# Kernel tuning notes

Measured on AMD Instinct MI355X. Metric: run time of the kernel, lower is better.

## Reference

```python
import jax, jax.numpy as jnp
import numpy as np

N = 50000      # nodes
E = 800000     # edges (before self-loops)
F_IN = 128
H = 4          # heads
C = 64         # per-head channels
G = 64         # graphs in batch
NEG_SLOPE = 0.2


def setup_inputs() -> dict:
    key = jax.random.key(0)
    ks = jax.random.split(key, 20)
    rn = lambda k, shape, s=0.1: (jax.random.normal(k, shape, jnp.float32) * s)
    x = jax.random.normal(ks[0], (N, F_IN), jnp.float32)
    edge_index = jax.random.randint(ks[1], (2, E), 0, N, dtype=jnp.int32)
    batch = jnp.sort(jax.random.randint(ks[2], (N,), 0, G, dtype=jnp.int32))
    return {
        "x": x, "edge_index": edge_index, "batch": batch,
        # layer 0: 128 -> (4 heads x 64), concat
        "W0": rn(ks[3], (F_IN, H * C)), "a_src0": rn(ks[4], (H, C)), "a_dst0": rn(ks[5], (H, C)), "b0": jnp.zeros((H * C,), jnp.float32),
        "W1": rn(ks[6], (H * C, H * C)), "a_src1": rn(ks[7], (H, C)), "a_dst1": rn(ks[8], (H, C)), "b1": jnp.zeros((H * C,), jnp.float32),
        "W2": rn(ks[9], (H * C, C)), "a_src2": rn(ks[10], (1, C)), "a_dst2": rn(ks[11], (1, C)), "b2": jnp.zeros((C,), jnp.float32),
        "lin_w": rn(ks[12], (C, 1)), "lin_b": jnp.zeros((1,), jnp.float32),
    }


def gat_layer(h_in, src, dst, W, a_src, a_dst, b, heads, ch, concat):
    n = h_in.shape[0]
    h = (h_in @ W).reshape(n, heads, ch)                         # [N,H,C]
    e_src = jnp.sum(h * a_src[None], axis=-1)                    # [N,H]
    e_dst = jnp.sum(h * a_dst[None], axis=-1)                    # [N,H]
    e = jax.nn.leaky_relu(e_src[src] + e_dst[dst], NEG_SLOPE)    # [E,H]
    # segment softmax over incoming edges of each destination node
    m = jax.ops.segment_max(e, dst, num_segments=n)
    m = jnp.where(jnp.isneginf(m), 0.0, m)
    ex = jnp.exp(e - m[dst])
    denom = jax.ops.segment_sum(ex, dst, num_segments=n)
    alpha = ex / (denom[dst] + 1e-16)                            # [E,H]
    out = jax.ops.segment_sum(h[src] * alpha[:, :, None], dst, num_segments=n)  # [N,H,C]
    out = out.reshape(n, heads * ch) if concat else out.mean(axis=1)
    return out + b


def reference(x, edge_index, batch, W0, a_src0, a_dst0, b0, W1, a_src1, a_dst1, b1, W2, a_src2, a_dst2, b2, lin_w, lin_b):
    n = x.shape[0]
    loops = jnp.arange(n, dtype=edge_index.dtype)
    src = jnp.concatenate([edge_index[0], loops])  # PyG add_self_loops=True
    dst = jnp.concatenate([edge_index[1], loops])
    h = jax.nn.relu(gat_layer(x, src, dst, W0, a_src0, a_dst0, b0, H, C, True))
    h = jax.nn.relu(gat_layer(h, src, dst, W1, a_src1, a_dst1, b1, H, C, True))
    h = gat_layer(h, src, dst, W2, a_src2, a_dst2, b2, 1, C, False)  # [N,64]
    # global mean pool per graph
    counts = jax.ops.segment_sum(jnp.ones((n,), h.dtype), batch, num_segments=G)
    pooled = jax.ops.segment_sum(h, batch, num_segments=G) / jnp.maximum(counts, 1.0)[:, None]
    return pooled @ lin_w + lin_b  # [G,1]
```

## Files before the change

### kernel.cpp

```cpp
#include <hip/hip_runtime.h>
#include <math.h>

typedef __bf16 bf16x8 __attribute__((ext_vector_type(8)));
typedef __bf16 bf16x4 __attribute__((ext_vector_type(4)));
typedef float f32x4 __attribute__((ext_vector_type(4)));
typedef float f32x2 __attribute__((ext_vector_type(2)));
typedef unsigned int u32x2 __attribute__((ext_vector_type(2)));
typedef unsigned int u32x4 __attribute__((ext_vector_type(4)));

#define LOG2E 1.4426950408889634f

static __device__ __forceinline__ float lrelu(float e) { return e > 0.0f ? e : 0.2f * e; }
static __device__ __forceinline__ float fexp2(float x) { return __builtin_amdgcn_exp2f(x); }

static __device__ __forceinline__ void dec16(u32x4 u, float* f) {
#pragma unroll
  for (int i = 0; i < 4; i++) {
    f32x2 a = __builtin_amdgcn_cvt_pk_f32_fp8(u[i], false);
    f32x2 b = __builtin_amdgcn_cvt_pk_f32_fp8(u[i], true);
    f[i * 4 + 0] = a.x;
    f[i * 4 + 1] = a.y;
    f[i * 4 + 2] = b.x;
    f[i * 4 + 3] = b.y;
  }
}

static __device__ __forceinline__ void dec8(unsigned int lo, unsigned int hi, float* f) {
  f32x2 a = __builtin_amdgcn_cvt_pk_f32_fp8(lo, false);
  f32x2 b = __builtin_amdgcn_cvt_pk_f32_fp8(lo, true);
  f32x2 c = __builtin_amdgcn_cvt_pk_f32_fp8(hi, false);
  f32x2 d = __builtin_amdgcn_cvt_pk_f32_fp8(hi, true);
  f[0] = a.x; f[1] = a.y; f[2] = b.x; f[3] = b.y;
  f[4] = c.x; f[5] = c.y; f[6] = d.x; f[7] = d.y;
}

static __device__ __forceinline__ int cmap(int p) {
  return (p & ~63) + (p & 3) * 16 + ((p & 63) >> 2);
}

__global__ void prep_kernel(const float* __restrict__ x, __bf16* __restrict__ xb, int n4,
                            const float* __restrict__ W0, __bf16* __restrict__ Bt0,
                            const float* __restrict__ W1, __bf16* __restrict__ Bt1,
                            const float* __restrict__ W2, __bf16* __restrict__ Bt2, int FIN,
                            int* __restrict__ cnt, int n) {
  int cb = (n4 + 255) / 256;
  int b = blockIdx.x;
  if (b < cb) {
    int i = b * 256 + threadIdx.x;
    if (i < n4) {
      f32x4 v = ((const f32x4*)x)[i];
      bf16x4 o = {(__bf16)v.x, (__bf16)v.y, (__bf16)v.z, (__bf16)v.w};
      ((bf16x4*)xb)[i] = o;
    }
    return;
  }
  b -= cb;
  if (b < 256) {
    for (int k = threadIdx.x; k < FIN; k += 256) Bt0[b * FIN + k] = (__bf16)W0[k * 256 + b];
    return;
  }
  b -= 256;
  if (b < 256) {
    int k = threadIdx.x;
    Bt1[b * 256 + k] = (__bf16)W1[cmap(k) * 256 + b];
    return;
  }
  b -= 256;
  if (b < 64) {
    int k = threadIdx.x;
    Bt2[b * 256 + k] = (__bf16)W2[cmap(k) * 64 + b];
    return;
  }
  b -= 64;
  int i = b * 256 + threadIdx.x;
  if (i < n) cnt[i] = 0;
}

template <int K, int NT>
__global__ __launch_bounds__(256) void count_gemm_kernel(
    const __bf16* __restrict__ A, const __bf16* __restrict__ Bt,
    const float* __restrict__ a_src, const float* __restrict__ a_dst,
    unsigned char* __restrict__ C, float* __restrict__ es, float* __restrict__ ed, int M,
    int gmx, const int* __restrict__ dst, int* __restrict__ cnt, int* __restrict__ rank, int E,
    int n) {
  constexpr int Nc = NT * 64;
  constexpr int H = NT;
  __shared__ __bf16 Bs[NT * 64][40];
  if ((int)blockIdx.x >= gmx) {
    int base = (blockIdx.x - gmx) * 1024 + threadIdx.x;
    int d4[4];
    bool ok[4];
#pragma unroll
    for (int t = 0; t < 4; t++) {
      int e = base + t * 256;
      ok[t] = (e < E + n);
      d4[t] = ok[t] ? ((e < E) ? dst[e] : (e - E)) : 0;
    }
#pragma unroll
    for (int t = 0; t < 4; t++)
      if (ok[t]) rank[base + t * 256] = atomicAdd(&cnt[d4[t]], 1);
    return;
  }
  int bid = blockIdx.x;
  int tid = threadIdx.x;
  int wave = tid >> 6;
  int lane = tid & 63;
  int quad = lane >> 4;
  int l16 = lane & 15;
  int rowBase = bid * 64 + wave * 16;
  f32x4 acc[NT * 4] = {};
  int arow = rowBase + l16;
  arow = (arow < M) ? arow : (M - 1);
  const __bf16* Aptr = &A[(size_t)arow * K + quad * 8];
  int sr = tid >> 2;
  int sc = (tid & 3) * 8;
  for (int kb = 0; kb < K; kb += 32) {
#pragma unroll
    for (int it = 0; it < NT; it++) {
      int r = it * 64 + sr;
      *(bf16x8*)&Bs[r][sc] = *(const bf16x8*)&Bt[(size_t)r * K + kb + sc];
    }
    __syncthreads();
    bf16x8 a = *(const bf16x8*)&Aptr[kb];
#pragma unroll
    for (int ng = 0; ng < NT * 4; ng++) {
      bf16x8 b = *(const bf16x8*)&Bs[ng * 16 + l16][quad * 8];
      acc[ng] = __builtin_amdgcn_mfma_f32_16x16x32_bf16(a, b, acc[ng], 0, 0, 0);
    }
    __syncthreads();
  }
  float asv[NT * 4], adv[NT * 4];
#pragma unroll
  for (int ng = 0; ng < NT * 4; ng++) {
    int c = (ng >> 2) * 64 + (ng & 3) * 16 + l16;
    asv[ng] = a_src[c];
    adv[ng] = a_dst[c];
  }
#pragma unroll
  for (int r = 0; r < 4; r++) {
    int row = rowBase + quad * 4 + r;
#pragma unroll
    for (int h = 0; h < H; h++) {
      float ss = 0.f, sd = 0.f;
#pragma unroll
      for (int g = 0; g < 4; g++) {
        float hv = acc[h * 4 + g][r];
        ss += hv * asv[h * 4 + g];
        sd += hv * adv[h * 4 + g];
      }
#pragma unroll
      for (int o = 1; o < 16; o <<= 1) {
        ss += __shfl_xor(ss, o);
        sd += __shfl_xor(sd, o);
      }
      if (row < M) {
        if (l16 == 0) {
          es[row * H + h] = ss * LOG2E;
          ed[row * H + h] = sd * LOG2E;
        }
        unsigned int pk = 0;
        pk = __builtin_amdgcn_cvt_pk_fp8_f32(acc[h * 4 + 0][r], acc[h * 4 + 1][r], pk, false);
        pk = __builtin_amdgcn_cvt_pk_fp8_f32(acc[h * 4 + 2][r], acc[h * 4 + 3][r], pk, true);
        *(unsigned int*)&C[(size_t)row * Nc + h * 64 + l16 * 4] = pk;
      }
    }
  }
}

__global__ __launch_bounds__(1024) void scan1_kernel(const int* __restrict__ counts,
                                                     int* __restrict__ offsets,
                                                     int* __restrict__ partials, int n) {
  __shared__ int sh[1024];
  int tid = threadIdx.x;
  int i = blockIdx.x * 1024 + tid;
  int v = (i < n) ? counts[i] : 0;
  sh[tid] = v;
  __syncthreads();
  for (int d = 1; d < 1024; d <<= 1) {
    int t = (tid >= d) ? sh[tid - d] : 0;
    __syncthreads();
    sh[tid] += t;
    __syncthreads();
  }
  if (i < n) offsets[i] = sh[tid] - v;
  if (tid == 1023) partials[blockIdx.x] = sh[1023];
}

__global__ __launch_bounds__(1024) void scan3_kernel(int* __restrict__ offsets,
                                                     const int* __restrict__ partials, int n,
                                                     int nb) {
  int lane = threadIdx.x & 63;
  int v = (lane < nb) ? partials[lane] : 0;
  int orig = v;
  for (int d = 1; d < 64; d <<= 1) {
    int t = __shfl_up(v, d);
    if (lane >= d) v += t;
  }
  int w = v - orig;
  int base = __shfl(w, blockIdx.x);
  int total = __shfl(v, 63);
  int i = blockIdx.x * 1024 + threadIdx.x;
  if (i < n) offsets[i] += base;
  if (blockIdx.x == 0 && threadIdx.x == 0) offsets[n] = total;
}

__global__ void scatter_kernel(const int* __restrict__ srcE, const int* __restrict__ dstE,
                               const int* __restrict__ offsets, const int* __restrict__ rank,
                               int* __restrict__ out_sorted, int E, int n) {
  int base = blockIdx.x * 1024 + threadIdx.x;
#pragma unroll
  for (int t = 0; t < 4; t++) {
    int e = base + t * 256;
    if (e < E + n) {
      int s = (e < E) ? srcE[e] : (e - E);
      int d = (e < E) ? dstE[e] : (e - E);
      out_sorted[offsets[d] + rank[e]] = s;
    }
  }
}

template <int K, int NT>
__global__ __launch_bounds__(256) void gemm2_kernel(const __bf16* __restrict__ A,
                                                    const __bf16* __restrict__ Bt,
                                                    const float* __restrict__ a_src,
                                                    const float* __restrict__ a_dst,
                                                    unsigned char* __restrict__ C,
                                                    float* __restrict__ es,
                                                    float* __restrict__ ed, int M) {
  constexpr int Nc = NT * 64;
  constexpr int H = NT;
  __shared__ __bf16 Bs[NT * 64][40];
  int tid = threadIdx.x;
  int wave = tid >> 6;
  int lane = tid & 63;
  int quad = lane >> 4;
  int l16 = lane & 15;
  int rowBase = blockIdx.x * 64 + wave * 16;
  f32x4 acc[NT * 4] = {};
  int arow = rowBase + l16;
  arow = (arow < M) ? arow : (M - 1);
  const __bf16* Aptr = &A[(size_t)arow * K + quad * 8];
  int sr = tid >> 2;
  int sc = (tid & 3) * 8;
  for (int kb = 0; kb < K; kb += 32) {
#pragma unroll
    for (int it = 0; it < NT; it++) {
      int r = it * 64 + sr;
      *(bf16x8*)&Bs[r][sc] = *(const bf16x8*)&Bt[(size_t)r * K + kb + sc];
    }
    __syncthreads();
    bf16x8 a = *(const bf16x8*)&Aptr[kb];
#pragma unroll
    for (int ng = 0; ng < NT * 4; ng++) {
      bf16x8 b = *(const bf16x8*)&Bs[ng * 16 + l16][quad * 8];
      acc[ng] = __builtin_amdgcn_mfma_f32_16x16x32_bf16(a, b, acc[ng], 0, 0, 0);
    }
    __syncthreads();
  }
  float asv[NT * 4], adv[NT * 4];
#pragma unroll
  for (int ng = 0; ng < NT * 4; ng++) {
    int c = (ng >> 2) * 64 + (ng & 3) * 16 + l16;
    asv[ng] = a_src[c];
    adv[ng] = a_dst[c];
  }
#pragma unroll
  for (int r = 0; r < 4; r++) {
    int row = rowBase + quad * 4 + r;
#pragma unroll
    for (int h = 0; h < H; h++) {
      float ss = 0.f, sd = 0.f;
#pragma unroll
      for (int g = 0; g < 4; g++) {
        float hv = acc[h * 4 + g][r];
        ss += hv * asv[h * 4 + g];
        sd += hv * adv[h * 4 + g];
      }
#pragma unroll
      for (int o = 1; o < 16; o <<= 1) {
        ss += __shfl_xor(ss, o);
        sd += __shfl_xor(sd, o);
      }
      if (row < M) {
        if (l16 == 0) {
          es[row * H + h] = ss * LOG2E;
          ed[row * H + h] = sd * LOG2E;
        }
        unsigned int pk = 0;
        pk = __builtin_amdgcn_cvt_pk_fp8_f32(acc[h * 4 + 0][r], acc[h * 4 + 1][r], pk, false);
        pk = __builtin_amdgcn_cvt_pk_fp8_f32(acc[h * 4 + 2][r], acc[h * 4 + 3][r], pk, true);
        *(unsigned int*)&C[(size_t)row * Nc + h * 64 + l16 * 4] = pk;
      }
    }
  }
}

__global__ void agg256_kernel(const unsigned char* __restrict__ h, const int* __restrict__ offsets,
                              const int* __restrict__ src_sorted, const float* __restrict__ es,
                              const float* __restrict__ ed, const float* __restrict__ bias,
                              __bf16* __restrict__ out, int n) {
  int node = blockIdx.x * (blockDim.x >> 6) + (threadIdx.x >> 6);
  int lane = threadIdx.x & 63;
  if (node >= n) return;
  int quad = lane >> 4;
  int l16 = lane & 15;
  int hd = l16 >> 2;
  float myEd = ed[node * 4 + hd];
  int off = offsets[node];
  int deg = offsets[node + 1] - off;
  float acc[16] = {};
  float sw = 0.f;
  int j = 0;
  int s0a = 0, s1a = 0;
  if (j + 8 <= deg) {
    s0a = src_sorted[off + j + quad];
    s1a = src_sorted[off + j + 4 + quad];
  }
  for (; j + 8 <= deg;) {
    int jn = j + 8;
    int s0 = s0a, s1 = s1a;
    if (jn + 8 <= deg) {
      s0a = src_sorted[off + jn + quad];
      s1a = src_sorted[off + jn + 4 + quad];
    }
    float e0 = es[s0 * 4 + hd];
    float e1 = es[s1 * 4 + hd];
    u32x4 u0 = *(const u32x4*)&h[(size_t)s0 * 256 + l16 * 16];
    u32x4 u1 = *(const u32x4*)&h[(size_t)s1 * 256 + l16 * 16];
    float w0 = fexp2(lrelu(e0 + myEd));
    float w1 = fexp2(lrelu(e1 + myEd));
    sw += w0 + w1;
    float f[16];
    dec16(u0, f);
#pragma unroll
    for (int k = 0; k < 16; k++) acc[k] += w0 * f[k];
    dec16(u1, f);
#pragma unroll
    for (int k = 0; k < 16; k++) acc[k] += w1 * f[k];
    j = jn;
  }
  for (; j < deg; j += 4) {
    if (quad < deg - j) {
      int s = src_sorted[off + j + quad];
      float w = fexp2(lrelu(es[s * 4 + hd] + myEd));
      sw += w;
      u32x4 u = *(const u32x4*)&h[(size_t)s * 256 + l16 * 16];
      float f[16];
      dec16(u, f);
#pragma unroll
      for (int k = 0; k < 16; k++) acc[k] += w * f[k];
    }
  }
  sw += __shfl_xor(sw, 16);
  sw += __shfl_xor(sw, 32);
#pragma unroll
  for (int k = 0; k < 16; k++) {
    acc[k] += __shfl_xor(acc[k], 16);
    acc[k] += __shfl_xor(acc[k], 32);
  }
  float invS = 1.0f / (sw + 1e-16f);
  if (quad == 0) {
    bf16x8 o0, o1;
#pragma unroll
    for (int k = 0; k < 16; k++) {
      int c = hd * 64 + (k & 3) * 16 + (l16 & 3) * 4 + (k >> 2);
      float v = fmaxf(acc[k] * invS + bias[c], 0.f);
      if (k < 8) o0[k] = (__bf16)v; else o1[k - 8] = (__bf16)v;
    }
    *(bf16x8*)&out[(size_t)node * 256 + l16 * 16] = o0;
    *(bf16x8*)&out[(size_t)node * 256 + l16 * 16 + 8] = o1;
  }
}

__global__ void agg64_kernel(const unsigned char* __restrict__ h, const int* __restrict__ offsets,
                             const int* __restrict__ src_sorted, const float* __restrict__ es,
                             const float* __restrict__ ed, const float* __restrict__ bias,
                             const float* __restrict__ lin_w, float* __restrict__ pnode, int n) {
  int node = blockIdx.x * (blockDim.x >> 6) + (threadIdx.x >> 6);
  int lane = threadIdx.x & 63;
  if (node >= n) return;
  int grp = lane >> 3;
  int l8 = lane & 7;
  float myEd = ed[node];
  int off = offsets[node];
  int deg = offsets[node + 1] - off;
  float acc[8] = {};
  float sw = 0.f;
  int j = 0;
  for (; j + 8 <= deg; j += 8) {
    int s = src_sorted[off + j + grp];
    float w = fexp2(lrelu(es[s] + myEd));
    sw += w;
    u32x2 u = *(const u32x2*)&h[(size_t)s * 64 + l8 * 8];
    float f[8];
    dec8(u.x, u.y, f);
#pragma unroll
    for (int k = 0; k < 8; k++) acc[k] += w * f[k];
  }
  if (j < deg && grp < deg - j) {
    int s = src_sorted[off + j + grp];
    float w = fexp2(lrelu(es[s] + myEd));
    sw += w;
    u32x2 u = *(const u32x2*)&h[(size_t)s * 64 + l8 * 8];
    float f[8];
    dec8(u.x, u.y, f);
#pragma unroll
    for (int k = 0; k < 8; k++) acc[k] += w * f[k];
  }
#pragma unroll
  for (int o = 8; o < 64; o <<= 1) {
    sw += __shfl_xor(sw, o);
#pragma unroll
    for (int k = 0; k < 8; k++) acc[k] += __shfl_xor(acc[k], o);
  }
  float invS = 1.0f / (sw + 1e-16f);
  float p = 0.f;
#pragma unroll
  for (int k = 0; k < 8; k++) {
    int c = (k & 3) * 16 + l8 * 2 + (k >> 2);
    p += (acc[k] * invS + bias[c]) * lin_w[c];
  }
#pragma unroll
  for (int o = 1; o < 8; o <<= 1) p += __shfl_xor(p, o);
  if (lane == 0) pnode[node] = p;
}

static __device__ __forceinline__ int lowerb(const int* __restrict__ a, int n, int key) {
  int lo = 0, hi = n;
  while (lo < hi) {
    int mid = (lo + hi) >> 1;
    if (a[mid] < key) lo = mid + 1; else hi = mid;
  }
  return lo;
}

__global__ void poolfinal_kernel(const float* __restrict__ pnode, const int* __restrict__ batch,
                                 const float* __restrict__ lin_b, float* __restrict__ out, int n) {
  __shared__ float ws[4];
  int g = blockIdx.x;
  int start = lowerb(batch, n, g);
  int end = lowerb(batch, n, g + 1);
  float acc = 0.f;
  for (int i = start + threadIdx.x; i < end; i += 256) acc += pnode[i];
  for (int o = 32; o > 0; o >>= 1) acc += __shfl_down(acc, o);
  if ((threadIdx.x & 63) == 0) ws[threadIdx.x >> 6] = acc;
  __syncthreads();
  if (threadIdx.x == 0) {
    float total = ws[0] + ws[1] + ws[2] + ws[3];
    out[g] = total / fmaxf((float)(end - start), 1.0f) + lin_b[0];
  }
}

extern "C" void kernel_launch(void* const* d_in, const int* in_sizes, int n_in, void* d_out,
                              int out_size, void* d_ws, size_t ws_size, hipStream_t stream) {
  const float* x = (const float*)d_in[0];
  const int* edge_index = (const int*)d_in[1];
  const int* batch = (const int*)d_in[2];
  const float* W0 = (const float*)d_in[3];
  const float* a_src0 = (const float*)d_in[4];
  const float* a_dst0 = (const float*)d_in[5];
  const float* b0 = (const float*)d_in[6];
  const float* W1 = (const float*)d_in[7];
  const float* a_src1 = (const float*)d_in[8];
  const float* a_dst1 = (const float*)d_in[9];
  const float* b1 = (const float*)d_in[10];
  const float* W2 = (const float*)d_in[11];
  const float* a_src2 = (const float*)d_in[12];
  const float* a_dst2 = (const float*)d_in[13];
  const float* b2 = (const float*)d_in[14];
  const float* lin_w = (const float*)d_in[15];
  const float* lin_b = (const float*)d_in[16];
  float* out = (float*)d_out;

  const int N = in_sizes[2];
  const int E = in_sizes[1] / 2;
  const int EE = E + N;
  const int G = 64;
  const int FIN = in_sizes[0] / N;

  const int* srcArr = edge_index;
  const int* dstArr = edge_index + E;

  size_t off = 0;
  auto alloc = [&](size_t bytes) -> void* {
    off = (off + 255) & ~(size_t)255;
    void* p = (char*)d_ws + off;
    off += bytes;
    return p;
  };
  __bf16* xb = (__bf16*)alloc((size_t)N * FIN * 2);
  unsigned char* hA = (unsigned char*)alloc((size_t)N * 256);
  __bf16* hB = (__bf16*)alloc((size_t)N * 256 * 2);
  unsigned char* h2 = (unsigned char*)alloc((size_t)N * 64);
  float* pnode = (float*)alloc((size_t)N * 4);
  __bf16* Bt0 = (__bf16*)alloc((size_t)256 * FIN * 2);
  __bf16* Bt1 = (__bf16*)alloc((size_t)256 * 256 * 2);
  __bf16* Bt2 = (__bf16*)alloc((size_t)64 * 256 * 2);
  float* es = (float*)alloc((size_t)N * 4 * 4);
  float* ed = (float*)alloc((size_t)N * 4 * 4);
  int* offsets = (int*)alloc((size_t)(N + 1) * 4);
  int* partials = (int*)alloc((size_t)64 * 4);
  int* rank = (int*)alloc((size_t)EE * 4);
  int* src_sorted = (int*)alloc((size_t)EE * 4);
  int* cnt = (int*)alloc((size_t)N * 4);
  (void)ws_size;

  int n4 = N * FIN / 4;
  int cb = (n4 + 255) / 256;
  int nz = (N + 255) / 256;
  int ebc4 = (EE + 1023) / 1024;
  int nb = (N + 1023) / 1024;
  int nwb = (N + 3) / 4;
  int gmx = (N + 63) / 64;

  prep_kernel<<<cb + 576 + nz, 256, 0, stream>>>(x, xb, n4, W0, Bt0, W1, Bt1, W2, Bt2, FIN, cnt,
                                                 N);

  count_gemm_kernel<128, 4><<<gmx + ebc4, 256, 0, stream>>>(
      xb, Bt0, a_src0, a_dst0, hA, es, ed, N, gmx, dstArr, cnt, rank, E, N);

  scan1_kernel<<<nb, 1024, 0, stream>>>(cnt, offsets, partials, N);
  scan3_kernel<<<nb, 1024, 0, stream>>>(offsets, partials, N, nb);
  scatter_kernel<<<ebc4, 256, 0, stream>>>(srcArr, dstArr, offsets, rank, src_sorted, E, N);

  agg256_kernel<<<nwb, 256, 0, stream>>>(hA, offsets, src_sorted, es, ed, b0, hB, N);

  gemm2_kernel<256, 4><<<gmx, 256, 0, stream>>>(hB, Bt1, a_src1, a_dst1, hA, es, ed, N);
  agg256_kernel<<<nwb, 256, 0, stream>>>(hA, offsets, src_sorted, es, ed, b1, hB, N);

  gemm2_kernel<256, 1><<<gmx, 256, 0, stream>>>(hB, Bt2, a_src2, a_dst2, h2, es, ed, N);
  agg64_kernel<<<nwb, 256, 0, stream>>>(h2, offsets, src_sorted, es, ed, b2, lin_w, pnode, N);

  poolfinal_kernel<<<G, 256, 0, stream>>>(pnode, batch, lin_b, out, N);
}
```

Before: 318.8 us.

## Build CSR with two-level bucket partition instead of count/scan/scatter

Edges are now partitioned into 256-node destination buckets. Each block builds a shared-memory histogram and does one global atomic per bucket, and a single bucket_csr kernel per bucket computes node offsets and writes the sorted sources. This replaces one global atomic per edge, the separate rank array, two scan kernels and a scatter kernel, cutting launches and random global traffic. Each bucket has a fixed capacity of 8192 entries with no overflow check, sources and local destinations are packed into 32 bits, and the partition buffer reuses the hB workspace.

```diff
diff --git a/kernel.cpp b/kernel.cpp
--- a/kernel.cpp
+++ b/kernel.cpp
@@ -9,6 +9,7 @@
 typedef unsigned int u32x4 __attribute__((ext_vector_type(4)));
 
 #define LOG2E 1.4426950408889634f
+#define BCAP 8192
 
 static __device__ __forceinline__ float lrelu(float e) { return e > 0.0f ? e : 0.2f * e; }
 static __device__ __forceinline__ float fexp2(float x) { return __builtin_amdgcn_exp2f(x); }
@@ -77,28 +78,46 @@
 }
 
 template <int K, int NT>
-__global__ __launch_bounds__(256) void count_gemm_kernel(
+__global__ __launch_bounds__(256) void gemm_part_kernel(
     const __bf16* __restrict__ A, const __bf16* __restrict__ Bt,
     const float* __restrict__ a_src, const float* __restrict__ a_dst,
     unsigned char* __restrict__ C, float* __restrict__ es, float* __restrict__ ed, int M,
-    int gmx, const int* __restrict__ dst, int* __restrict__ cnt, int* __restrict__ rank, int E,
-    int n) {
+    int gmx, const int* __restrict__ srcE, const int* __restrict__ dstE,
+    int* __restrict__ bucket_cnt, unsigned int* __restrict__ part, int E, int EE, int n) {
   constexpr int Nc = NT * 64;
   constexpr int H = NT;
   __shared__ __bf16 Bs[NT * 64][40];
   if ((int)blockIdx.x >= gmx) {
-    int base = (blockIdx.x - gmx) * 1024 + threadIdx.x;
-    int d4[4];
-    bool ok[4];
-#pragma unroll
-    for (int t = 0; t < 4; t++) {
-      int e = base + t * 256;
-      ok[t] = (e < E + n);
-      d4[t] = ok[t] ? ((e < E) ? dst[e] : (e - E)) : 0;
-    }
-#pragma unroll
-    for (int t = 0; t < 4; t++)
-      if (ok[t]) rank[base + t * 256] = atomicAdd(&cnt[d4[t]], 1);
+    int tid = threadIdx.x;
+    int* hist = (int*)&Bs[0][0];
+    int* gbase = hist + 256;
+    hist[tid] = 0;
+    __syncthreads();
+    int ab = ((int)blockIdx.x - gmx) * 4096;
+    int sv[16], dv[16];
+#pragma unroll
+    for (int t = 0; t < 16; t++) {
+      int e = ab + t * 256 + tid;
+      if (e < EE) {
+        if (e < E) { sv[t] = srcE[e]; dv[t] = dstE[e]; }
+        else { sv[t] = dv[t] = e - E; }
+      } else { sv[t] = -1; dv[t] = 0; }
+    }
+    int lr[16];
+#pragma unroll
+    for (int t = 0; t < 16; t++)
+      if (sv[t] >= 0) lr[t] = atomicAdd(&hist[dv[t] >> 8], 1);
+    __syncthreads();
+    int NB = (n + 255) >> 8;
+    gbase[tid] = (tid < NB && hist[tid] > 0) ? atomicAdd(&bucket_cnt[tid * 16], hist[tid]) : 0;
+    __syncthreads();
+#pragma unroll
+    for (int t = 0; t < 16; t++)
+      if (sv[t] >= 0) {
+        int bk = dv[t] >> 8;
+        part[(size_t)bk * BCAP + gbase[bk] + lr[t]] =
+            (unsigned int)sv[t] | ((unsigned int)(dv[t] & 255) << 24);
+      }
     return;
   }
   int bid = blockIdx.x;
@@ -167,55 +186,54 @@
   }
 }
 
-__global__ __launch_bounds__(1024) void scan1_kernel(const int* __restrict__ counts,
-                                                     int* __restrict__ offsets,
-                                                     int* __restrict__ partials, int n) {
-  __shared__ int sh[1024];
+__global__ __launch_bounds__(1024) void bucket_csr_kernel(
+    const unsigned int* __restrict__ part, const int* __restrict__ bucket_cnt,
+    int* __restrict__ offsets, int* __restrict__ src_sorted, int n, int EE) {
+  __shared__ int sc[256];
+  __shared__ int excl[256];
+  __shared__ int run[256];
   int tid = threadIdx.x;
-  int i = blockIdx.x * 1024 + tid;
-  int v = (i < n) ? counts[i] : 0;
-  sh[tid] = v;
+  int b = blockIdx.x;
+  int NB = (n + 255) >> 8;
+  if (tid < 256) sc[tid] = (tid < NB) ? bucket_cnt[tid * 16] : 0;
   __syncthreads();
-  for (int d = 1; d < 1024; d <<= 1) {
-    int t = (tid >= d) ? sh[tid - d] : 0;
-    __syncthreads();
-    sh[tid] += t;
-    __syncthreads();
-  }
-  if (i < n) offsets[i] = sh[tid] - v;
-  if (tid == 1023) partials[blockIdx.x] = sh[1023];
-}
-
-__global__ __launch_bounds__(1024) void scan3_kernel(int* __restrict__ offsets,
-                                                     const int* __restrict__ partials, int n,
-                                                     int nb) {
-  int lane = threadIdx.x & 63;
-  int v = (lane < nb) ? partials[lane] : 0;
-  int orig = v;
-  for (int d = 1; d < 64; d <<= 1) {
-    int t = __shfl_up(v, d);
-    if (lane >= d) v += t;
-  }
-  int w = v - orig;
-  int base = __shfl(w, blockIdx.x);
-  int total = __shfl(v, 63);
-  int i = blockIdx.x * 1024 + threadIdx.x;
-  if (i < n) offsets[i] += base;
-  if (blockIdx.x == 0 && threadIdx.x == 0) offsets[n] = total;
-}
-
-__global__ void scatter_kernel(const int* __restrict__ srcE, const int* __restrict__ dstE,
-                               const int* __restrict__ offsets, const int* __restrict__ rank,
-                               int* __restrict__ out_sorted, int E, int n) {
-  int base = blockIdx.x * 1024 + threadIdx.x;
-#pragma unroll
-  for (int t = 0; t < 4; t++) {
-    int e = base + t * 256;
-    if (e < E + n) {
-      int s = (e < E) ? srcE[e] : (e - E);
-      int d = (e < E) ? dstE[e] : (e - E);
-      out_sorted[offsets[d] + rank[e]] = s;
-    }
+  for (int d = 1; d < 256; d <<= 1) {
+    int t = 0;
+    if (tid < 256 && tid >= d) t = sc[tid - d];
+    __syncthreads();
+    if (tid < 256) sc[tid] += t;
+    __syncthreads();
+  }
+  int base = (b == 0) ? 0 : sc[b - 1];
+  int cb = sc[b] - base;
+  const unsigned int* mypart = part + (size_t)b * BCAP;
+  if (tid < 256) run[tid] = 0;
+  __syncthreads();
+  for (int i = tid; i < cb; i += 1024) atomicAdd(&run[mypart[i] >> 24], 1);
+  __syncthreads();
+  int myc = (tid < 256) ? run[tid] : 0;
+  if (tid < 256) sc[tid] = myc;
+  __syncthreads();
+  for (int d = 1; d < 256; d <<= 1) {
+    int t = 0;
+    if (tid < 256 && tid >= d) t = sc[tid - d];
+    __syncthreads();
+    if (tid < 256) sc[tid] += t;
+    __syncthreads();
+  }
+  if (tid < 256) {
+    excl[tid] = sc[tid] - myc;
+    int node = b * 256 + tid;
+    if (node < n) offsets[node] = base + excl[tid];
+    run[tid] = 0;
+  }
+  if (b == 0 && tid == 0) offsets[n] = EE;
+  __syncthreads();
+  for (int i = tid; i < cb; i += 1024) {
+    unsigned int p = mypart[i];
+    int j = p >> 24;
+    int r = atomicAdd(&run[j], 1);
+    src_sorted[base + excl[j] + r] = (int)(p & 0xFFFFFFu);
   }
 }
 
@@ -499,29 +517,27 @@
   float* es = (float*)alloc((size_t)N * 4 * 4);
   float* ed = (float*)alloc((size_t)N * 4 * 4);
   int* offsets = (int*)alloc((size_t)(N + 1) * 4);
-  int* partials = (int*)alloc((size_t)64 * 4);
-  int* rank = (int*)alloc((size_t)EE * 4);
   int* src_sorted = (int*)alloc((size_t)EE * 4);
-  int* cnt = (int*)alloc((size_t)N * 4);
+  int* bucket_cnt = (int*)alloc((size_t)4096 * 4);
   (void)ws_size;
+
+  int NB = (N + 255) >> 8;
+
+  unsigned int* part = (unsigned int*)hB;
 
   int n4 = N * FIN / 4;
   int cb = (n4 + 255) / 256;
-  int nz = (N + 255) / 256;
-  int ebc4 = (EE + 1023) / 1024;
-  int nb = (N + 1023) / 1024;
   int nwb = (N + 3) / 4;
   int gmx = (N + 63) / 64;
-
-  prep_kernel<<<cb + 576 + nz, 256, 0, stream>>>(x, xb, n4, W0, Bt0, W1, Bt1, W2, Bt2, FIN, cnt,
-                                                 N);
-
-  count_gemm_kernel<128, 4><<<gmx + ebc4, 256, 0, stream>>>(
-      xb, Bt0, a_src0, a_dst0, hA, es, ed, N, gmx, dstArr, cnt, rank, E, N);
-
-  scan1_kernel<<<nb, 1024, 0, stream>>>(cnt, offsets, partials, N);
-  scan3_kernel<<<nb, 1024, 0, stream>>>(offsets, partials, N, nb);
-  scatter_kernel<<<ebc4, 256, 0, stream>>>(srcArr, dstArr, offsets, rank, src_sorted, E, N);
+  int nA = (EE + 4095) / 4096;
+
+  prep_kernel<<<cb + 576 + 16, 256, 0, stream>>>(x, xb, n4, W0, Bt0, W1, Bt1, W2, Bt2, FIN,
+                                                 bucket_cnt, 4096);
+
+  gemm_part_kernel<128, 4><<<gmx + nA, 256, 0, stream>>>(
+      xb, Bt0, a_src0, a_dst0, hA, es, ed, N, gmx, srcArr, dstArr, bucket_cnt, part, E, EE, N);
+
+  bucket_csr_kernel<<<NB, 1024, 0, stream>>>(part, bucket_cnt, offsets, src_sorted, N, EE);
 
   agg256_kernel<<<nwb, 256, 0, stream>>>(hA, offsets, src_sorted, es, ed, b0, hB, N);
 
```

Result: faster. 288.4 us (-9.5%).
